# Kernel tuning notes

Measured on AMD Instinct MI355X. Metric: run time of the kernel, lower is better.

Reference implementation:

```python
import jax, jax.numpy as jnp
import numpy as np

H = 8
D = 512
DK = D // H
B = 16
N = 8192


def setup_inputs() -> dict:
    key = jax.random.key(0)
    k1, k2, k3, k4 = jax.random.split(key, 4)
    x = jax.random.normal(k1, (B, N, D), dtype=jnp.float32)
    W_k = jax.random.normal(k2, (D, D), dtype=jnp.float32) * (1.0 / np.sqrt(D))
    W_g = jax.random.normal(k3, (D, D), dtype=jnp.float32) * (1.0 / np.sqrt(D))
    query = jax.random.normal(k4, (H, 1, DK), dtype=jnp.float32)
    return {"x": x, "W_k": W_k, "W_g": W_g, "query": query}


def reference(x, W_k, W_g, query):
    b, n, d = x.shape
    # nn.Linear: y = x @ W.T  (no bias)
    K = (x @ W_k.T).reshape(b, n, H, DK).transpose(0, 2, 1, 3)  # (b,h,n,dk)
    G = (x @ W_g.T).reshape(b, n, H, DK).transpose(0, 2, 1, 3)  # (b,h,n,dk)
    xh = x.reshape(b, n, H, DK).transpose(0, 2, 1, 3)           # (b,h,n,dk)
    gated = jnp.tanh(K) * jax.nn.sigmoid(G)                     # (b,h,n,dk)
    # single-query attention: scores (b,h,1,n)
    scores = jnp.einsum('hmd,bhnd->bhmn', query, gated)
    attn = jax.nn.softmax(scores, axis=-1)
    out = jnp.einsum('bhmn,bhnd->bhmd', attn, xh)               # (b,h,1,dk)
    out = out.transpose(0, 2, 1, 3).reshape(b, 1, H * DK)
    return out.squeeze()  # (b, d)
```

## Files before the change

kernel.cpp:

```cpp
#include <hip/hip_runtime.h>
#include <hip/hip_bf16.h>

#define H_ 8
#define D_ 512
#define DK_ 64
#define B_ 16
#define N_ 8192
#define M_ (B_ * N_)

typedef __attribute__((ext_vector_type(8))) short short8;
typedef __attribute__((ext_vector_type(4))) float floatx4;

__device__ __forceinline__ void glds16(const void* g, void* l) {
    __builtin_amdgcn_global_load_lds((const __attribute__((address_space(1))) void*)g,
                                     (__attribute__((address_space(3))) void*)l,
                                     16, 0, 0);
}

__device__ __forceinline__ unsigned short f2bf(float f) {
    unsigned u = __float_as_uint(f);
    return (unsigned short)((u + 0x7fffu + ((u >> 16) & 1u)) >> 16);
}

__device__ __forceinline__ unsigned pack_bf2(float x, float y) {
    return __builtin_amdgcn_perm(__float_as_uint(y) + 0x8000u,
                                 __float_as_uint(x) + 0x8000u, 0x07060302u);
}

__device__ __forceinline__ short8 pack_bf8(float4 lo, float4 hi) {
    union { unsigned u[4]; short8 s; } tmp;
    tmp.u[0] = pack_bf2(lo.x, lo.y);
    tmp.u[1] = pack_bf2(lo.z, lo.w);
    tmp.u[2] = pack_bf2(hi.x, hi.y);
    tmp.u[3] = pack_bf2(hi.z, hi.w);
    return tmp.s;
}

__global__ __launch_bounds__(256) void cvt2_kernel(const float* __restrict__ s0,
                                                   const float* __restrict__ s1,
                                                   unsigned short* __restrict__ d0,
                                                   unsigned short* __restrict__ d1) {
    const int blk = blockIdx.x;
    const float* src = (blk < 256) ? s0 : s1;
    unsigned short* dst = (blk < 256) ? d0 : d1;
    int i = (blk & 255) * 256 + threadIdx.x;
    float4 v = ((const float4*)src)[i];
    ushort4 o;
    o.x = f2bf(v.x); o.y = f2bf(v.y); o.z = f2bf(v.z); o.w = f2bf(v.w);
    ((ushort4*)dst)[i] = o;
}

__global__ __launch_bounds__(256, 2) void gemm_score_kernel(
    const float* __restrict__ x,
    const unsigned short* __restrict__ wkb,
    const unsigned short* __restrict__ wgb,
    const float* __restrict__ query,
    float* __restrict__ s_buf)
{
    __shared__ unsigned short lds[6][128 * 32];

    const int t = threadIdx.x;
    const int lane = t & 63;
    const int wave = t >> 6;
    const int wm = wave >> 1, wn = wave & 1;

    const int g = blockIdx.x;
    const int xcd = g & 7;
    const int s = g >> 3;
    const int jt = s & 3;
    const int mt = ((s >> 2) << 3) | xcd;
    const int jc = jt * 128;
    const int m0 = mt * 128;

    floatx4 acc_k[4][4], acc_g[4][4];
#pragma unroll
    for (int i = 0; i < 4; ++i)
#pragma unroll
        for (int j = 0; j < 4; ++j) { acc_k[i][j] = (floatx4)0.f; acc_g[i][j] = (floatx4)0.f; }

    const int ar = t >> 1;
    const int ac0 = (t & 1) * 2;
    const int aswr = (ar >> 1) & 3;
    const float* pA = x + (size_t)(m0 + ar) * 512 + (t & 1) * 16;
    const int ao0 = (ar * 4 + (ac0 ^ aswr)) * 8;
    const int ao1 = (ar * 4 + ((ac0 + 1) ^ aswr)) * 8;

    int boff[2];
#pragma unroll
    for (int i = 0; i < 2; ++i) {
        int p = i * 256 + t;
        int r = p >> 2;
        int c = (p & 3) ^ ((r >> 1) & 3);
        boff[i] = (jc + r) * 512 + c * 8;
    }

    const int fr = lane & 15;
    const int q  = lane >> 4;
    const int slq = (q ^ ((fr >> 1) & 3)) * 8;

#pragma unroll
    for (int i = 0; i < 2; ++i) {
        glds16(wkb + boff[i], &lds[2][(i * 256 + t) * 8]);
        glds16(wgb + boff[i], &lds[4][(i * 256 + t) * 8]);
    }
    {
        float4 f0 = *(const float4*)(pA + 0);
        float4 f1 = *(const float4*)(pA + 4);
        float4 f2 = *(const float4*)(pA + 8);
        float4 f3 = *(const float4*)(pA + 12);
        *(short8*)&lds[0][ao0] = pack_bf8(f0, f1);
        *(short8*)&lds[0][ao1] = pack_bf8(f2, f3);
    }
    __syncthreads();

#pragma unroll
    for (int k = 0; k < 16; ++k) {
        const int cur = k & 1, nxt = cur ^ 1;
        float4 f0, f1, f2, f3;
        if (k < 15) {
            const int k1 = (k + 1) * 32;
#pragma unroll
            for (int i = 0; i < 2; ++i) {
                glds16(wkb + boff[i] + k1, &lds[2 + nxt][(i * 256 + t) * 8]);
                glds16(wgb + boff[i] + k1, &lds[4 + nxt][(i * 256 + t) * 8]);
            }
            f0 = *(const float4*)(pA + k1 + 0);
            f1 = *(const float4*)(pA + k1 + 4);
            f2 = *(const float4*)(pA + k1 + 8);
            f3 = *(const float4*)(pA + k1 + 12);
        }

        short8 a[4], bk[4], bg[4];
#pragma unroll
        for (int mi = 0; mi < 4; ++mi)
            a[mi] = *(const short8*)(&lds[cur][(wm * 64 + mi * 16 + fr) * 32 + slq]);
#pragma unroll
        for (int ni = 0; ni < 4; ++ni) {
            bk[ni] = *(const short8*)(&lds[2 + cur][(wn * 64 + ni * 16 + fr) * 32 + slq]);
            bg[ni] = *(const short8*)(&lds[4 + cur][(wn * 64 + ni * 16 + fr) * 32 + slq]);
        }
#pragma unroll
        for (int mi = 0; mi < 4; ++mi)
#pragma unroll
            for (int ni = 0; ni < 4; ++ni) {
                acc_k[mi][ni] = __builtin_amdgcn_mfma_f32_16x16x32_bf16(a[mi], bk[ni], acc_k[mi][ni], 0, 0, 0);
                acc_g[mi][ni] = __builtin_amdgcn_mfma_f32_16x16x32_bf16(a[mi], bg[ni], acc_g[mi][ni], 0, 0, 0);
            }

        if (k < 15) {
            *(short8*)&lds[nxt][ao0] = pack_bf8(f0, f1);
            *(short8*)&lds[nxt][ao1] = pack_bf8(f2, f3);
            __syncthreads();
        }
    }

    const int h = jt * 2 + wn;
    float qv[4];
#pragma unroll
    for (int ni = 0; ni < 4; ++ni) qv[ni] = query[h * 64 + ni * 16 + fr];

#pragma unroll
    for (int mi = 0; mi < 4; ++mi) {
#pragma unroll
        for (int r = 0; r < 4; ++r) {
            float v = 0.f;
#pragma unroll
            for (int ni = 0; ni < 4; ++ni) {
                float kv = acc_k[mi][ni][r];
                float gv = acc_g[mi][ni][r];
                float e2k = __expf(2.f * kv);
                float th = 1.f - 2.f / (e2k + 1.f);
                float sg = 1.f / (1.f + __expf(-gv));
                v += qv[ni] * th * sg;
            }
            v += __shfl_xor(v, 1);
            v += __shfl_xor(v, 2);
            v += __shfl_xor(v, 4);
            v += __shfl_xor(v, 8);
            if (fr == 0) {
                int mg = m0 + wm * 64 + mi * 16 + (lane >> 4) * 4 + r;
                int b = mg >> 13, n = mg & 8191;
                s_buf[((size_t)(b * 8 + h) << 13) + n] = v;
            }
        }
    }
}

__global__ __launch_bounds__(256) void stats_kernel(const float* __restrict__ s_buf,
                                                    float* __restrict__ mb, float* __restrict__ lb) {
    const int bh = blockIdx.x;
    const float* s = s_buf + ((size_t)bh << 13);
    const int t = threadIdx.x;
    float mx = -3.0e38f;
    for (int i = t; i < 8192; i += 256) mx = fmaxf(mx, s[i]);
#pragma unroll
    for (int m = 32; m > 0; m >>= 1) mx = fmaxf(mx, __shfl_xor(mx, m));
    __shared__ float red[8];
    if ((t & 63) == 0) red[t >> 6] = mx;
    __syncthreads();
    mx = fmaxf(fmaxf(red[0], red[1]), fmaxf(red[2], red[3]));
    float sum = 0.f;
    for (int i = t; i < 8192; i += 256) sum += __expf(s[i] - mx);
#pragma unroll
    for (int m = 32; m > 0; m >>= 1) sum += __shfl_xor(sum, m);
    if ((t & 63) == 0) red[4 + (t >> 6)] = sum;
    __syncthreads();
    if (t == 0) { mb[bh] = mx; lb[bh] = red[4] + red[5] + red[6] + red[7]; }
}

__global__ __launch_bounds__(256) void out_part_kernel(
    const float* __restrict__ x, const float* __restrict__ s_buf,
    const float* __restrict__ mb, const float* __restrict__ lb,
    float* __restrict__ part) {
    const int b = blockIdx.x >> 5;
    const int chunk = blockIdx.x & 31;
    const int n0 = chunk * 256;
    const int t = threadIdx.x;
    __shared__ float w[8 * 256];
    for (int i = t; i < 2048; i += 256) {
        int hh = i >> 8, nn = i & 255;
        int bh = b * 8 + hh;
        w[i] = __expf(s_buf[((size_t)bh << 13) + n0 + nn] - mb[bh]) / lb[bh];
    }
    __syncthreads();
    const int rg = t >> 6;
    const int d0 = (t & 63) * 8;
    const float* wh = w + ((d0 >> 6) << 8);
    float acc[8] = {0.f, 0.f, 0.f, 0.f, 0.f, 0.f, 0.f, 0.f};
    for (int nn = rg; nn < 256; nn += 4) {
        const float4* row = (const float4*)(x + (((size_t)(b * 8192 + n0 + nn)) << 9) + d0);
        float4 v0 = row[0];
        float4 v1 = row[1];
        float ww = wh[nn];
        acc[0] += ww * v0.x; acc[1] += ww * v0.y;
        acc[2] += ww * v0.z; acc[3] += ww * v0.w;
        acc[4] += ww * v1.x; acc[5] += ww * v1.y;
        acc[6] += ww * v1.z; acc[7] += ww * v1.w;
    }
    float* dst = part + ((size_t)(blockIdx.x * 4 + rg)) * 512 + d0;
    *(float4*)(dst)     = make_float4(acc[0], acc[1], acc[2], acc[3]);
    *(float4*)(dst + 4) = make_float4(acc[4], acc[5], acc[6], acc[7]);
}

__global__ __launch_bounds__(512) void out_reduce_kernel(const float* __restrict__ part,
                                                         float* __restrict__ out) {
    const int b = blockIdx.x;
    const int d = threadIdx.x;
    float s = 0.f;
    const float* p = part + (size_t)b * 128 * 512 + d;
    for (int i = 0; i < 128; ++i) s += p[(size_t)i * 512];
    out[b * 512 + d] = s;
}

extern "C" void kernel_launch(void* const* d_in, const int* in_sizes, int n_in,
                              void* d_out, int out_size, void* d_ws, size_t ws_size,
                              hipStream_t stream) {
    const float* x  = (const float*)d_in[0];
    const float* Wk = (const float*)d_in[1];
    const float* Wg = (const float*)d_in[2];
    const float* q  = (const float*)d_in[3];
    float* out = (float*)d_out;

    char* ws = (char*)d_ws;
    unsigned short* wkb = (unsigned short*)ws;
    unsigned short* wgb = (unsigned short*)(ws + 524288ull);
    float* s_buf = (float*)(ws + 1048576ull);
    float* part  = (float*)(ws + 5242880ull);
    float* mb = (float*)(ws + 9437184ull);
    float* lb = (float*)(ws + 9437696ull);

    hipLaunchKernelGGL(cvt2_kernel, dim3(512), dim3(256), 0, stream, Wk, Wg, wkb, wgb);
    hipLaunchKernelGGL(gemm_score_kernel, dim3(4096), dim3(256), 0, stream, x, wkb, wgb, q, s_buf);
    hipLaunchKernelGGL(stats_kernel, dim3(128), dim3(256), 0, stream, s_buf, mb, lb);
    hipLaunchKernelGGL(out_part_kernel, dim3(512), dim3(256), 0, stream, x, s_buf, mb, lb, part);
    hipLaunchKernelGGL(out_reduce_kernel, dim3(16), dim3(512), 0, stream, part, out);
}
```

Baseline: 621.5 us.

## Retile score GEMM to one head per block with wider K step

Each block of the fused K/G GEMM now covers 64 output columns (one attention head) instead of 128. The grid doubles and the per-thread accumulators halve, aiming to reduce register pressure and allow three blocks per CU. The K step widens from 32 to 64 with an XOR swizzle over 8 chunks, and the double-buffered prefetch is replaced by a single-buffered load-sync-compute loop. The two column-half waves combine their score partials through shared memory before one store. In exchange, each x tile is read and converted to bf16 by twice as many blocks, and global-load latency is no longer overlapped with MFMA work inside a block.

Result: slower. 641.4 us (+3.2%).

```diff
diff --git a/kernel.cpp b/kernel.cpp
--- a/kernel.cpp
+++ b/kernel.cpp
@@ -50,14 +50,17 @@
     ((ushort4*)dst)[i] = o;
 }
 
-__global__ __launch_bounds__(256, 2) void gemm_score_kernel(
+__global__ __launch_bounds__(256, 3) void gemm_score_kernel(
     const float* __restrict__ x,
     const unsigned short* __restrict__ wkb,
     const unsigned short* __restrict__ wgb,
     const float* __restrict__ query,
     float* __restrict__ s_buf)
 {
-    __shared__ unsigned short lds[6][128 * 32];
+    __shared__ unsigned short lds_a[128 * 64];
+    __shared__ unsigned short lds_k[64 * 64];
+    __shared__ unsigned short lds_g[64 * 64];
+    __shared__ float sred[2][128];
 
     const int t = threadIdx.x;
     const int lane = t & 63;
@@ -67,97 +70,84 @@
     const int g = blockIdx.x;
     const int xcd = g & 7;
     const int s = g >> 3;
-    const int jt = s & 3;
-    const int mt = ((s >> 2) << 3) | xcd;
-    const int jc = jt * 128;
+    const int h = s & 7;
+    const int mt = ((s >> 3) << 3) | xcd;
     const int m0 = mt * 128;
-
-    floatx4 acc_k[4][4], acc_g[4][4];
+    const int jc = h * 64;
+
+    floatx4 acc_k[4][2], acc_g[4][2];
 #pragma unroll
     for (int i = 0; i < 4; ++i)
 #pragma unroll
-        for (int j = 0; j < 4; ++j) { acc_k[i][j] = (floatx4)0.f; acc_g[i][j] = (floatx4)0.f; }
+        for (int j = 0; j < 2; ++j) { acc_k[i][j] = (floatx4)0.f; acc_g[i][j] = (floatx4)0.f; }
 
     const int ar = t >> 1;
-    const int ac0 = (t & 1) * 2;
-    const int aswr = (ar >> 1) & 3;
-    const float* pA = x + (size_t)(m0 + ar) * 512 + (t & 1) * 16;
-    const int ao0 = (ar * 4 + (ac0 ^ aswr)) * 8;
-    const int ao1 = (ar * 4 + ((ac0 + 1) ^ aswr)) * 8;
+    const int ah = t & 1;
+    const float4* pA4 = (const float4*)(x + (size_t)(m0 + ar) * 512 + ah * 32);
+    int ao[4];
+#pragma unroll
+    for (int j = 0; j < 4; ++j) ao[j] = (ar * 8 + ((ah * 4 + j) ^ (ar & 7))) * 8;
 
     int boff[2];
 #pragma unroll
     for (int i = 0; i < 2; ++i) {
         int p = i * 256 + t;
-        int r = p >> 2;
-        int c = (p & 3) ^ ((r >> 1) & 3);
+        int r = p >> 3;
+        int c = (p & 7) ^ (r & 7);
         boff[i] = (jc + r) * 512 + c * 8;
     }
 
     const int fr = lane & 15;
     const int q  = lane >> 4;
-    const int slq = (q ^ ((fr >> 1) & 3)) * 8;
-
-#pragma unroll
-    for (int i = 0; i < 2; ++i) {
-        glds16(wkb + boff[i], &lds[2][(i * 256 + t) * 8]);
-        glds16(wgb + boff[i], &lds[4][(i * 256 + t) * 8]);
-    }
-    {
-        float4 f0 = *(const float4*)(pA + 0);
-        float4 f1 = *(const float4*)(pA + 4);
-        float4 f2 = *(const float4*)(pA + 8);
-        float4 f3 = *(const float4*)(pA + 12);
-        *(short8*)&lds[0][ao0] = pack_bf8(f0, f1);
-        *(short8*)&lds[0][ao1] = pack_bf8(f2, f3);
-    }
-    __syncthreads();
-
-#pragma unroll
-    for (int k = 0; k < 16; ++k) {
-        const int cur = k & 1, nxt = cur ^ 1;
-        float4 f0, f1, f2, f3;
-        if (k < 15) {
-            const int k1 = (k + 1) * 32;
-#pragma unroll
-            for (int i = 0; i < 2; ++i) {
-                glds16(wkb + boff[i] + k1, &lds[2 + nxt][(i * 256 + t) * 8]);
-                glds16(wgb + boff[i] + k1, &lds[4 + nxt][(i * 256 + t) * 8]);
+    const int sw = fr & 7;
+
+    for (int k = 0; k < 8; ++k) {
+        const int k0 = k * 64;
+        float4 af0 = pA4[k * 16 + 0];
+        float4 af1 = pA4[k * 16 + 1];
+        float4 af2 = pA4[k * 16 + 2];
+        float4 af3 = pA4[k * 16 + 3];
+        float4 af4 = pA4[k * 16 + 4];
+        float4 af5 = pA4[k * 16 + 5];
+        float4 af6 = pA4[k * 16 + 6];
+        float4 af7 = pA4[k * 16 + 7];
+#pragma unroll
+        for (int i = 0; i < 2; ++i) {
+            glds16(wkb + boff[i] + k0, &lds_k[(i * 256 + t) * 8]);
+            glds16(wgb + boff[i] + k0, &lds_g[(i * 256 + t) * 8]);
+        }
+        *(short8*)&lds_a[ao[0]] = pack_bf8(af0, af1);
+        *(short8*)&lds_a[ao[1]] = pack_bf8(af2, af3);
+        *(short8*)&lds_a[ao[2]] = pack_bf8(af4, af5);
+        *(short8*)&lds_a[ao[3]] = pack_bf8(af6, af7);
+        __syncthreads();
+
+#pragma unroll
+        for (int kc = 0; kc < 2; ++kc) {
+            const int sl = ((kc * 4 + q) ^ sw) * 8;
+            short8 a[4], bk[2], bg[2];
+#pragma unroll
+            for (int mi = 0; mi < 4; ++mi)
+                a[mi] = *(const short8*)(&lds_a[(wm * 64 + mi * 16 + fr) * 64 + sl]);
+#pragma unroll
+            for (int ni = 0; ni < 2; ++ni) {
+                bk[ni] = *(const short8*)(&lds_k[(wn * 32 + ni * 16 + fr) * 64 + sl]);
+                bg[ni] = *(const short8*)(&lds_g[(wn * 32 + ni * 16 + fr) * 64 + sl]);
             }
-            f0 = *(const float4*)(pA + k1 + 0);
-            f1 = *(const float4*)(pA + k1 + 4);
-            f2 = *(const float4*)(pA + k1 + 8);
-            f3 = *(const float4*)(pA + k1 + 12);
+#pragma unroll
+            for (int mi = 0; mi < 4; ++mi)
+#pragma unroll
+                for (int ni = 0; ni < 2; ++ni) {
+                    acc_k[mi][ni] = __builtin_amdgcn_mfma_f32_16x16x32_bf16(a[mi], bk[ni], acc_k[mi][ni], 0, 0, 0);
+                    acc_g[mi][ni] = __builtin_amdgcn_mfma_f32_16x16x32_bf16(a[mi], bg[ni], acc_g[mi][ni], 0, 0, 0);
+                }
         }
-
-        short8 a[4], bk[4], bg[4];
-#pragma unroll
-        for (int mi = 0; mi < 4; ++mi)
-            a[mi] = *(const short8*)(&lds[cur][(wm * 64 + mi * 16 + fr) * 32 + slq]);
-#pragma unroll
-        for (int ni = 0; ni < 4; ++ni) {
-            bk[ni] = *(const short8*)(&lds[2 + cur][(wn * 64 + ni * 16 + fr) * 32 + slq]);
-            bg[ni] = *(const short8*)(&lds[4 + cur][(wn * 64 + ni * 16 + fr) * 32 + slq]);
-        }
-#pragma unroll
-        for (int mi = 0; mi < 4; ++mi)
-#pragma unroll
-            for (int ni = 0; ni < 4; ++ni) {
-                acc_k[mi][ni] = __builtin_amdgcn_mfma_f32_16x16x32_bf16(a[mi], bk[ni], acc_k[mi][ni], 0, 0, 0);
-                acc_g[mi][ni] = __builtin_amdgcn_mfma_f32_16x16x32_bf16(a[mi], bg[ni], acc_g[mi][ni], 0, 0, 0);
-            }
-
-        if (k < 15) {
-            *(short8*)&lds[nxt][ao0] = pack_bf8(f0, f1);
-            *(short8*)&lds[nxt][ao1] = pack_bf8(f2, f3);
-            __syncthreads();
-        }
-    }
-
-    const int h = jt * 2 + wn;
-    float qv[4];
-#pragma unroll
-    for (int ni = 0; ni < 4; ++ni) qv[ni] = query[h * 64 + ni * 16 + fr];
+        __syncthreads();
+    }
+
+    float qv[2];
+#pragma unroll
+    for (int ni = 0; ni < 2; ++ni) qv[ni] = query[h * 64 + wn * 32 + ni * 16 + fr];
 
 #pragma unroll
     for (int mi = 0; mi < 4; ++mi) {
@@ -165,7 +155,7 @@
         for (int r = 0; r < 4; ++r) {
             float v = 0.f;
 #pragma unroll
-            for (int ni = 0; ni < 4; ++ni) {
+            for (int ni = 0; ni < 2; ++ni) {
                 float kv = acc_k[mi][ni][r];
                 float gv = acc_g[mi][ni][r];
                 float e2k = __expf(2.f * kv);
@@ -177,12 +167,15 @@
             v += __shfl_xor(v, 2);
             v += __shfl_xor(v, 4);
             v += __shfl_xor(v, 8);
-            if (fr == 0) {
-                int mg = m0 + wm * 64 + mi * 16 + (lane >> 4) * 4 + r;
-                int b = mg >> 13, n = mg & 8191;
-                s_buf[((size_t)(b * 8 + h) << 13) + n] = v;
-            }
+            if (fr == 0) sred[wn][wm * 64 + mi * 16 + q * 4 + r] = v;
         }
+    }
+    __syncthreads();
+    if (t < 128) {
+        float v = sred[0][t] + sred[1][t];
+        int mg = m0 + t;
+        int b = mg >> 13, n = mg & 8191;
+        s_buf[((size_t)(b * 8 + h) << 13) + n] = v;
     }
 }
 
@@ -270,7 +263,7 @@
     float* lb = (float*)(ws + 9437696ull);
 
     hipLaunchKernelGGL(cvt2_kernel, dim3(512), dim3(256), 0, stream, Wk, Wg, wkb, wgb);
-    hipLaunchKernelGGL(gemm_score_kernel, dim3(4096), dim3(256), 0, stream, x, wkb, wgb, q, s_buf);
+    hipLaunchKernelGGL(gemm_score_kernel, dim3(8192), dim3(256), 0, stream, x, wkb, wgb, q, s_buf);
     hipLaunchKernelGGL(stats_kernel, dim3(128), dim3(256), 0, stream, s_buf, mb, lb);
     hipLaunchKernelGGL(out_part_kernel, dim3(512), dim3(256), 0, stream, x, s_buf, mb, lb, part);
     hipLaunchKernelGGL(out_reduce_kernel, dim3(16), dim3(512), 0, stream, part, out);
```

## Restructure score GEMM per head, load A directly from global, drop weight conversion

Applied to the files above, without the earlier changes.

Each block now handles 256 rows for one head, and each wave owns 64 rows. The head's 64 Wk and Wg rows are converted from fp32 to bf16 straight into padded LDS in two K-halves. A fragments are read from global fp32 into registers and packed there, so x no longer goes through LDS or double buffering. This removes the separate weight conversion kernel and most barriers. In exchange, every block re-converts its weight slices, x loads are strided with no latency hiding between MFMA steps, and the global-to-LDS async loads are gone.

After: 796.6 us. 28.2% more time.

```diff
diff --git a/kernel.cpp b/kernel.cpp
--- a/kernel.cpp
+++ b/kernel.cpp
@@ -10,17 +10,6 @@
 
 typedef __attribute__((ext_vector_type(8))) short short8;
 typedef __attribute__((ext_vector_type(4))) float floatx4;
-
-__device__ __forceinline__ void glds16(const void* g, void* l) {
-    __builtin_amdgcn_global_load_lds((const __attribute__((address_space(1))) void*)g,
-                                     (__attribute__((address_space(3))) void*)l,
-                                     16, 0, 0);
-}
-
-__device__ __forceinline__ unsigned short f2bf(float f) {
-    unsigned u = __float_as_uint(f);
-    return (unsigned short)((u + 0x7fffu + ((u >> 16) & 1u)) >> 16);
-}
 
 __device__ __forceinline__ unsigned pack_bf2(float x, float y) {
     return __builtin_amdgcn_perm(__float_as_uint(y) + 0x8000u,
@@ -36,125 +25,88 @@
     return tmp.s;
 }
 
-__global__ __launch_bounds__(256) void cvt2_kernel(const float* __restrict__ s0,
-                                                   const float* __restrict__ s1,
-                                                   unsigned short* __restrict__ d0,
-                                                   unsigned short* __restrict__ d1) {
-    const int blk = blockIdx.x;
-    const float* src = (blk < 256) ? s0 : s1;
-    unsigned short* dst = (blk < 256) ? d0 : d1;
-    int i = (blk & 255) * 256 + threadIdx.x;
-    float4 v = ((const float4*)src)[i];
-    ushort4 o;
-    o.x = f2bf(v.x); o.y = f2bf(v.y); o.z = f2bf(v.z); o.w = f2bf(v.w);
-    ((ushort4*)dst)[i] = o;
-}
-
 __global__ __launch_bounds__(256, 2) void gemm_score_kernel(
     const float* __restrict__ x,
-    const unsigned short* __restrict__ wkb,
-    const unsigned short* __restrict__ wgb,
+    const float* __restrict__ Wk,
+    const float* __restrict__ Wg,
     const float* __restrict__ query,
     float* __restrict__ s_buf)
 {
-    __shared__ unsigned short lds[6][128 * 32];
+    __shared__ unsigned short ldsW[2][64 * 264];
 
     const int t = threadIdx.x;
     const int lane = t & 63;
     const int wave = t >> 6;
-    const int wm = wave >> 1, wn = wave & 1;
 
     const int g = blockIdx.x;
     const int xcd = g & 7;
     const int s = g >> 3;
-    const int jt = s & 3;
-    const int mt = ((s >> 2) << 3) | xcd;
-    const int jc = jt * 128;
-    const int m0 = mt * 128;
+    const int h = s & 7;
+    const int mc = ((s >> 3) << 3) | xcd;
+    const int m0 = mc * 256;
 
     floatx4 acc_k[4][4], acc_g[4][4];
 #pragma unroll
     for (int i = 0; i < 4; ++i)
 #pragma unroll
         for (int j = 0; j < 4; ++j) { acc_k[i][j] = (floatx4)0.f; acc_g[i][j] = (floatx4)0.f; }
-
-    const int ar = t >> 1;
-    const int ac0 = (t & 1) * 2;
-    const int aswr = (ar >> 1) & 3;
-    const float* pA = x + (size_t)(m0 + ar) * 512 + (t & 1) * 16;
-    const int ao0 = (ar * 4 + (ac0 ^ aswr)) * 8;
-    const int ao1 = (ar * 4 + ((ac0 + 1) ^ aswr)) * 8;
-
-    int boff[2];
-#pragma unroll
-    for (int i = 0; i < 2; ++i) {
-        int p = i * 256 + t;
-        int r = p >> 2;
-        int c = (p & 3) ^ ((r >> 1) & 3);
-        boff[i] = (jc + r) * 512 + c * 8;
-    }
 
     const int fr = lane & 15;
     const int q  = lane >> 4;
-    const int slq = (q ^ ((fr >> 1) & 3)) * 8;
-
-#pragma unroll
-    for (int i = 0; i < 2; ++i) {
-        glds16(wkb + boff[i], &lds[2][(i * 256 + t) * 8]);
-        glds16(wgb + boff[i], &lds[4][(i * 256 + t) * 8]);
-    }
-    {
-        float4 f0 = *(const float4*)(pA + 0);
-        float4 f1 = *(const float4*)(pA + 4);
-        float4 f2 = *(const float4*)(pA + 8);
-        float4 f3 = *(const float4*)(pA + 12);
-        *(short8*)&lds[0][ao0] = pack_bf8(f0, f1);
-        *(short8*)&lds[0][ao1] = pack_bf8(f2, f3);
-    }
-    __syncthreads();
-
-#pragma unroll
-    for (int k = 0; k < 16; ++k) {
-        const int cur = k & 1, nxt = cur ^ 1;
-        float4 f0, f1, f2, f3;
-        if (k < 15) {
-            const int k1 = (k + 1) * 32;
-#pragma unroll
-            for (int i = 0; i < 2; ++i) {
-                glds16(wkb + boff[i] + k1, &lds[2 + nxt][(i * 256 + t) * 8]);
-                glds16(wgb + boff[i] + k1, &lds[4 + nxt][(i * 256 + t) * 8]);
-            }
-            f0 = *(const float4*)(pA + k1 + 0);
-            f1 = *(const float4*)(pA + k1 + 4);
-            f2 = *(const float4*)(pA + k1 + 8);
-            f3 = *(const float4*)(pA + k1 + 12);
+
+    const float* pA[4];
+#pragma unroll
+    for (int mi = 0; mi < 4; ++mi)
+        pA[mi] = x + (size_t)(m0 + wave * 64 + mi * 16 + fr) * 512 + q * 8;
+
+    int bo[4];
+#pragma unroll
+    for (int ni = 0; ni < 4; ++ni) bo[ni] = (ni * 16 + fr) * 264 + q * 8;
+
+    const float* wkRow = Wk + (size_t)h * 64 * 512;
+    const float* wgRow = Wg + (size_t)h * 64 * 512;
+
+    for (int ph = 0; ph < 2; ++ph) {
+        if (ph) __syncthreads();
+#pragma unroll
+        for (int i = 0; i < 8; ++i) {
+            int j = i * 256 + t;
+            int row = j >> 5, c8 = j & 31;
+            size_t so = (size_t)row * 512 + ph * 256 + c8 * 8;
+            float4 k0 = *(const float4*)(wkRow + so);
+            float4 k1 = *(const float4*)(wkRow + so + 4);
+            float4 g0 = *(const float4*)(wgRow + so);
+            float4 g1 = *(const float4*)(wgRow + so + 4);
+            *(short8*)&ldsW[0][row * 264 + c8 * 8] = pack_bf8(k0, k1);
+            *(short8*)&ldsW[1][row * 264 + c8 * 8] = pack_bf8(g0, g1);
         }
-
-        short8 a[4], bk[4], bg[4];
-#pragma unroll
-        for (int mi = 0; mi < 4; ++mi)
-            a[mi] = *(const short8*)(&lds[cur][(wm * 64 + mi * 16 + fr) * 32 + slq]);
-#pragma unroll
-        for (int ni = 0; ni < 4; ++ni) {
-            bk[ni] = *(const short8*)(&lds[2 + cur][(wn * 64 + ni * 16 + fr) * 32 + slq]);
-            bg[ni] = *(const short8*)(&lds[4 + cur][(wn * 64 + ni * 16 + fr) * 32 + slq]);
+        __syncthreads();
+
+        const int kb = ph * 256;
+#pragma unroll
+        for (int kt = 0; kt < 8; ++kt) {
+            short8 a[4], bk[4], bg[4];
+#pragma unroll
+            for (int mi = 0; mi < 4; ++mi) {
+                float4 f0 = *(const float4*)(pA[mi] + kb + kt * 32);
+                float4 f1 = *(const float4*)(pA[mi] + kb + kt * 32 + 4);
+                a[mi] = pack_bf8(f0, f1);
+            }
+#pragma unroll
+            for (int ni = 0; ni < 4; ++ni) {
+                bk[ni] = *(const short8*)&ldsW[0][bo[ni] + kt * 32];
+                bg[ni] = *(const short8*)&ldsW[1][bo[ni] + kt * 32];
+            }
+#pragma unroll
+            for (int mi = 0; mi < 4; ++mi)
+#pragma unroll
+                for (int ni = 0; ni < 4; ++ni) {
+                    acc_k[mi][ni] = __builtin_amdgcn_mfma_f32_16x16x32_bf16(a[mi], bk[ni], acc_k[mi][ni], 0, 0, 0);
+                    acc_g[mi][ni] = __builtin_amdgcn_mfma_f32_16x16x32_bf16(a[mi], bg[ni], acc_g[mi][ni], 0, 0, 0);
+                }
         }
-#pragma unroll
-        for (int mi = 0; mi < 4; ++mi)
-#pragma unroll
-            for (int ni = 0; ni < 4; ++ni) {
-                acc_k[mi][ni] = __builtin_amdgcn_mfma_f32_16x16x32_bf16(a[mi], bk[ni], acc_k[mi][ni], 0, 0, 0);
-                acc_g[mi][ni] = __builtin_amdgcn_mfma_f32_16x16x32_bf16(a[mi], bg[ni], acc_g[mi][ni], 0, 0, 0);
-            }
-
-        if (k < 15) {
-            *(short8*)&lds[nxt][ao0] = pack_bf8(f0, f1);
-            *(short8*)&lds[nxt][ao1] = pack_bf8(f2, f3);
-            __syncthreads();
-        }
-    }
-
-    const int h = jt * 2 + wn;
+    }
+
     float qv[4];
 #pragma unroll
     for (int ni = 0; ni < 4; ++ni) qv[ni] = query[h * 64 + ni * 16 + fr];
@@ -178,7 +130,7 @@
             v += __shfl_xor(v, 4);
             v += __shfl_xor(v, 8);
             if (fr == 0) {
-                int mg = m0 + wm * 64 + mi * 16 + (lane >> 4) * 4 + r;
+                int mg = m0 + wave * 64 + mi * 16 + q * 4 + r;
                 int b = mg >> 13, n = mg & 8191;
                 s_buf[((size_t)(b * 8 + h) << 13) + n] = v;
             }
@@ -262,15 +214,12 @@
     float* out = (float*)d_out;
 
     char* ws = (char*)d_ws;
-    unsigned short* wkb = (unsigned short*)ws;
-    unsigned short* wgb = (unsigned short*)(ws + 524288ull);
-    float* s_buf = (float*)(ws + 1048576ull);
-    float* part  = (float*)(ws + 5242880ull);
-    float* mb = (float*)(ws + 9437184ull);
-    float* lb = (float*)(ws + 9437696ull);
-
-    hipLaunchKernelGGL(cvt2_kernel, dim3(512), dim3(256), 0, stream, Wk, Wg, wkb, wgb);
-    hipLaunchKernelGGL(gemm_score_kernel, dim3(4096), dim3(256), 0, stream, x, wkb, wgb, q, s_buf);
+    float* s_buf = (float*)ws;
+    float* part  = (float*)(ws + 4194304ull);
+    float* mb = (float*)(ws + 8388608ull);
+    float* lb = (float*)(ws + 8389120ull);
+
+    hipLaunchKernelGGL(gemm_score_kernel, dim3(4096), dim3(256), 0, stream, x, Wk, Wg, q, s_buf);
     hipLaunchKernelGGL(stats_kernel, dim3(128), dim3(256), 0, stream, s_buf, mb, lb);
     hipLaunchKernelGGL(out_part_kernel, dim3(512), dim3(256), 0, stream, x, s_buf, mb, lb, part);
     hipLaunchKernelGGL(out_reduce_kernel, dim3(16), dim3(512), 0, stream, part, out);
```
